# Kernel tuning notes

Hardware: AMD Instinct MI355X
Metric: run time of the kernel (lower is better)

The kernel has to match this reference:

```python
import jax, jax.numpy as jnp
import numpy as np


def setup_inputs() -> dict:
    key = jax.random.key(0)
    ks = jax.random.split(key, 8)
    B = 65536
    scale = lambda fan_in: 1.0 / np.sqrt(fan_in)
    return {
        "x": jax.random.normal(ks[0], (B, 784), dtype=jnp.float32),
        "w0": jax.random.normal(ks[1], (124, 784), dtype=jnp.float32) * scale(784),
        "w1": jax.random.normal(ks[2], (32, 124), dtype=jnp.float32) * scale(124),
        "w3": jax.random.normal(ks[3], (22, 32), dtype=jnp.float32) * scale(32),
        "b3": jax.random.normal(ks[4], (22,), dtype=jnp.float32) * scale(32),
        "w5": jax.random.normal(ks[5], (21, 22), dtype=jnp.float32) * scale(22),
        "b5": jax.random.normal(ks[6], (21,), dtype=jnp.float32) * scale(22),
        "w7": jax.random.normal(ks[7], (10, 21), dtype=jnp.float32) * scale(21),
    }


def reference(x, w0, w1, w3, b3, w5, b5, w7):
    # x: [B, 784]; PyTorch Linear: y = x @ W.T (+ b)
    h = x @ w0.T                       # [B, 124] (no bias, no activation)
    h = jax.nn.relu(h @ w1.T)          # [B, 32]
    h = jax.nn.relu(h @ w3.T + b3)     # [B, 22]
    h = jax.nn.relu(h @ w5.T + b5)     # [B, 21]
    logits = h @ w7.T                  # [B, 10]
    return jax.nn.log_softmax(logits, axis=1)
```

## Files before the change

kernel.cpp:

```cpp
#include <hip/hip_runtime.h>
#include <hip/hip_fp16.h>

typedef _Float16 half8 __attribute__((ext_vector_type(8)));
typedef __fp16 cvt2_t __attribute__((ext_vector_type(2)));
typedef float f32x4 __attribute__((ext_vector_type(4)));

#define W0F_UNITS (13 * 1024)
#define W1F_OFF   (W0F_UNITS * 16)
#define W1F_UNITS 512
#define SW_OFF    (W1F_OFF + W1F_UNITS * 16)

#define L_H0   0
#define L_H1   8192
#define L_H3   0
#define L_H5   3200
#define L_OS   6400
#define LDS_SZ 10240

__global__ void prep_weights(const float* __restrict__ w0,
                             const float* __restrict__ w1,
                             const float* __restrict__ w3,
                             const float* __restrict__ b3,
                             const float* __restrict__ w5,
                             const float* __restrict__ b5,
                             const float* __restrict__ w7,
                             char* __restrict__ ws) {
  int tid = blockIdx.x * 256 + threadIdx.x;
  if (tid < W0F_UNITS) {
    int t  = tid >> 10;
    int kf = (tid >> 9) & 1;
    int nf = (tid >> 6) & 7;
    int l  = tid & 63;
    int n  = nf * 16 + (l & 15);
    int k0 = t * 64 + kf * 32 + (l >> 4) * 8;
    alignas(16) __half h[8];
#pragma unroll
    for (int e = 0; e < 8; e++) {
      int k = k0 + e;
      h[e] = __float2half((n < 124 && k < 784) ? w0[n * 784 + k] : 0.f);
    }
    *(uint4*)(ws + tid * 16) = *(const uint4*)h;
    return;
  }
  int r = tid - W0F_UNITS;
  if (r < W1F_UNITS) {
    int kf = r >> 7;
    int nf = (r >> 6) & 1;
    int l  = r & 63;
    int n  = nf * 16 + (l & 15);
    int k0 = kf * 32 + (l >> 4) * 8;
    alignas(16) __half h[8];
#pragma unroll
    for (int e = 0; e < 8; e++) {
      int k = k0 + e;
      h[e] = __float2half((k < 124) ? w1[n * 124 + k] : 0.f);
    }
    *(uint4*)(ws + W1F_OFF + r * 16) = *(const uint4*)h;
    return;
  }
  r -= W1F_UNITS;
  float* sw = (float*)(ws + SW_OFF);
  if (r < 704) { sw[r] = w3[r]; return; }
  r -= 704;
  if (r < 504) {
    int n = r / 24, k = r % 24;
    sw[704 + r] = (k < 22) ? w5[n * 22 + k] : 0.f;
    return;
  }
  r -= 504;
  if (r < 240) {
    int n = r / 24, k = r % 24;
    sw[1208 + r] = (k < 21) ? w7[n * 21 + k] : 0.f;
    return;
  }
  r -= 240;
  if (r < 24) { sw[1448 + r] = (r < 22) ? b3[r] : 0.f; return; }
  r -= 24;
  if (r < 24) { sw[1472 + r] = (r < 21) ? b5[r] : 0.f; return; }
}

__device__ __forceinline__ half8 cvt8(const f32x4& a, const f32x4& b) {
  cvt2_t p0 = __builtin_amdgcn_cvt_pkrtz(a[0], a[1]);
  cvt2_t p1 = __builtin_amdgcn_cvt_pkrtz(a[2], a[3]);
  cvt2_t p2 = __builtin_amdgcn_cvt_pkrtz(b[0], b[1]);
  cvt2_t p3 = __builtin_amdgcn_cvt_pkrtz(b[2], b[3]);
  uint4 u;
  u.x = __builtin_bit_cast(unsigned, p0);
  u.y = __builtin_bit_cast(unsigned, p1);
  u.z = __builtin_bit_cast(unsigned, p2);
  u.w = __builtin_bit_cast(unsigned, p3);
  return __builtin_bit_cast(half8, u);
}

__global__ __launch_bounds__(64, 2) void fused_mlp(
    const float* __restrict__ x, const char* __restrict__ ws,
    float* __restrict__ out) {
  __shared__ alignas(16) char sm[LDS_SZ];
  const int l  = threadIdx.x;
  const int lr = l & 15;
  const int lg = l >> 4;
  const size_t row0 = (size_t)blockIdx.x * 32;
  const uint4* wf = (const uint4*)ws;

  const float* xb0 = x + (row0 + lr) * 784;
  const float* xb1 = xb0 + 16 * 784;

  f32x4 acc[2][8];
#pragma unroll
  for (int mf = 0; mf < 2; mf++)
#pragma unroll
    for (int nf = 0; nf < 8; nf++) acc[mf][nf] = f32x4{0.f, 0.f, 0.f, 0.f};

  f32x4 xr[2][4][2];
  half8 afr[2][4];
  half8 bfr[2][8];

#define XL(T, G)                                                               \
  {                                                                            \
    _Pragma("unroll") for (int mf = 0; mf < 2; mf++)                           \
        _Pragma("unroll") for (int kf = 0; kf < 4; kf++)                       \
            _Pragma("unroll") for (int h = 0; h < 2; h++) {                    \
      const float* p =                                                         \
          (mf ? xb1 : xb0) + (T) * 128 + kf * 32 + lg * 8 + h * 4;             \
      if (!(G) || (kf == 0 && lg < 2))                                         \
        xr[mf][kf][h] = *(const f32x4*)p;                                      \
      else                                                                     \
        xr[mf][kf][h] = f32x4{0.f, 0.f, 0.f, 0.f};                             \
    }                                                                          \
  }

#define CVALL()                                                                \
  {                                                                            \
    _Pragma("unroll") for (int mf = 0; mf < 2; mf++)                           \
        _Pragma("unroll") for (int kf = 0; kf < 4; kf++)                       \
            afr[mf][kf] = cvt8(xr[mf][kf][0], xr[mf][kf][1]);                  \
  }

#define BFL(P, G)                                                              \
  {                                                                            \
    _Pragma("unroll") for (int nf = 0; nf < 8; nf++)                           \
      bfr[P][nf] = __builtin_bit_cast(                                         \
          half8, wf[((G) >> 1) * 1024 + ((G) & 1) * 512 + nf * 64 + l]);       \
  }

#define MFK(KF, P)                                                             \
  {                                                                            \
    _Pragma("unroll") for (int nf = 0; nf < 8; nf++) {                         \
      acc[0][nf] = __builtin_amdgcn_mfma_f32_16x16x32_f16(                     \
          afr[0][KF], bfr[P][nf], acc[0][nf], 0, 0, 0);                        \
      acc[1][nf] = __builtin_amdgcn_mfma_f32_16x16x32_f16(                     \
          afr[1][KF], bfr[P][nf], acc[1][nf], 0, 0, 0);                        \
    }                                                                          \
  }

#define BODY(T, GN)                                                            \
  {                                                                            \
    CVALL()                                                                    \
    XL((T) + 1, GN)                                                            \
    MFK(0, 0)                                                                  \
    BFL(0, (T) * 4 + 2)                                                        \
    MFK(1, 1)                                                                  \
    BFL(1, (T) * 4 + 3)                                                        \
    MFK(2, 0)                                                                  \
    BFL(0, ((T) + 1) * 4 + 0)                                                  \
    MFK(3, 1)                                                                  \
    BFL(1, ((T) + 1) * 4 + 1)                                                  \
  }

  XL(0, 0)
  BFL(0, 0)
  BFL(1, 1)

  BODY(0, 0)
  BODY(1, 0)
  BODY(2, 0)
  BODY(3, 0)
  BODY(4, 0)
  BODY(5, 1)
  CVALL()
  MFK(0, 0)

  half8 b1[4][2];
  {
    const uint4* w1f = (const uint4*)(ws + W1F_OFF);
#pragma unroll
    for (int kf = 0; kf < 4; kf++)
#pragma unroll
      for (int nf = 0; nf < 2; nf++)
        b1[kf][nf] = __builtin_bit_cast(half8, w1f[kf * 128 + nf * 64 + l]);
  }

#pragma unroll
  for (int mf = 0; mf < 2; mf++)
#pragma unroll
    for (int nf = 0; nf < 8; nf++)
#pragma unroll
      for (int q = 0; q < 4; q++) {
        int rr = mf * 16 + lg * 4 + q;
        int cc = nf * 16 + lr;
        *(__half*)(sm + L_H0 + rr * 256 + ((2 * cc) ^ ((rr & 7) << 4))) =
            __float2half(acc[mf][nf][q]);
      }
  __syncthreads();

  f32x4 acc1[2][2];
#pragma unroll
  for (int mf = 0; mf < 2; mf++) {
    acc1[mf][0] = f32x4{0.f, 0.f, 0.f, 0.f};
    acc1[mf][1] = f32x4{0.f, 0.f, 0.f, 0.f};
  }
#pragma unroll
  for (int kf = 0; kf < 4; kf++) {
    half8 a1[2];
#pragma unroll
    for (int mf = 0; mf < 2; mf++) {
      int rr = mf * 16 + lr;
      int cb = kf * 64 + lg * 16;
      a1[mf] = *(const half8*)(sm + L_H0 + rr * 256 + (cb ^ ((rr & 7) << 4)));
    }
#pragma unroll
    for (int mf = 0; mf < 2; mf++)
#pragma unroll
      for (int nf = 0; nf < 2; nf++)
        acc1[mf][nf] = __builtin_amdgcn_mfma_f32_16x16x32_f16(
            a1[mf], b1[kf][nf], acc1[mf][nf], 0, 0, 0);
  }
#pragma unroll
  for (int mf = 0; mf < 2; mf++)
#pragma unroll
    for (int nf = 0; nf < 2; nf++)
#pragma unroll
      for (int q = 0; q < 4; q++) {
        int rr = mf * 16 + lg * 4 + q;
        int cc = nf * 16 + lr;
        float v = fmaxf(acc1[mf][nf][q], 0.f);
        *(__half*)(sm + L_H1 + rr * 64 + ((2 * cc) ^ ((rr & 3) << 4))) =
            __float2half(v);
      }
  __syncthreads();

  const int r = l & 31;
  const int j = l >> 5;
  float h1v[32];
#pragma unroll
  for (int cb = 0; cb < 4; cb++) {
    half8 v = *(const half8*)(sm + L_H1 + r * 64 + ((cb * 16) ^ ((r & 3) << 4)));
#pragma unroll
    for (int e = 0; e < 8; e++) h1v[cb * 8 + e] = (float)v[e];
  }
  const float* w3g = (const float*)(ws + SW_OFF);
  const float* w5g = (const float*)(ws + SW_OFF + 2816);
  const float* w7g = (const float*)(ws + SW_OFF + 4832);
  const float* b3g = (const float*)(ws + SW_OFF + 5792);
  const float* b5g = (const float*)(ws + SW_OFF + 5888);
  float* h3l = (float*)(sm + L_H3);
  float* h5l = (float*)(sm + L_H5);

#pragma unroll
  for (int i = 0; i < 11; i++) {
    int n = j + 2 * i;
    float s = b3g[n];
    const float4* wrow = (const float4*)(w3g + n * 32);
#pragma unroll
    for (int kk = 0; kk < 8; kk++) {
      float4 wv = wrow[kk];
      s += h1v[4 * kk] * wv.x + h1v[4 * kk + 1] * wv.y +
           h1v[4 * kk + 2] * wv.z + h1v[4 * kk + 3] * wv.w;
    }
    h3l[r * 25 + n] = fmaxf(s, 0.f);
  }
  __syncthreads();
  float h3v[24];
#pragma unroll
  for (int k = 0; k < 24; k++) h3v[k] = (k < 22) ? h3l[r * 25 + k] : 0.f;
#pragma unroll
  for (int i = 0; i < 11; i++) {
    int n = j + 2 * i;
    if (n < 21) {
      float s = b5g[n];
      const float4* wrow = (const float4*)(w5g + n * 24);
#pragma unroll
      for (int kk = 0; kk < 6; kk++) {
        float4 wv = wrow[kk];
        s += h3v[4 * kk] * wv.x + h3v[4 * kk + 1] * wv.y +
             h3v[4 * kk + 2] * wv.z + h3v[4 * kk + 3] * wv.w;
      }
      h5l[r * 25 + n] = fmaxf(s, 0.f);
    }
  }
  __syncthreads();
  if (j == 0) {
    float h5v[24];
#pragma unroll
    for (int k = 0; k < 24; k++) h5v[k] = (k < 21) ? h5l[r * 25 + k] : 0.f;
    float lgt[10];
    float mx = -3.4e38f;
#pragma unroll
    for (int n = 0; n < 10; n++) {
      float s = 0.f;
      const float4* wrow = (const float4*)(w7g + n * 24);
#pragma unroll
      for (int kk = 0; kk < 6; kk++) {
        float4 wv = wrow[kk];
        s += h5v[4 * kk] * wv.x + h5v[4 * kk + 1] * wv.y +
             h5v[4 * kk + 2] * wv.z + h5v[4 * kk + 3] * wv.w;
      }
      lgt[n] = s;
      mx = fmaxf(mx, s);
    }
    float se = 0.f;
#pragma unroll
    for (int n = 0; n < 10; n++) se += __expf(lgt[n] - mx);
    const float lse = mx + __logf(se);
    float* os = (float*)(sm + L_OS);
#pragma unroll
    for (int n = 0; n < 10; n++) os[r * 10 + n] = lgt[n] - lse;
  }
  __syncthreads();
  {
    const float* os = (const float*)(sm + L_OS);
#pragma unroll
    for (int i = 0; i < 5; i++) out[row0 * 10 + i * 64 + l] = os[i * 64 + l];
  }
}

extern "C" void kernel_launch(void* const* d_in, const int* in_sizes, int n_in,
                              void* d_out, int out_size, void* d_ws, size_t ws_size,
                              hipStream_t stream) {
  const float* x  = (const float*)d_in[0];
  const float* w0 = (const float*)d_in[1];
  const float* w1 = (const float*)d_in[2];
  const float* w3 = (const float*)d_in[3];
  const float* b3 = (const float*)d_in[4];
  const float* w5 = (const float*)d_in[5];
  const float* b5 = (const float*)d_in[6];
  const float* w7 = (const float*)d_in[7];
  float* out = (float*)d_out;
  char* ws = (char*)d_ws;

  const int prep_threads = W0F_UNITS + W1F_UNITS + 704 + 504 + 240 + 24 + 24;
  prep_weights<<<(prep_threads + 255) / 256, 256, 0, stream>>>(w0, w1, w3, b3,
                                                               w5, b5, w7, ws);
  fused_mlp<<<65536 / 32, 64, 0, stream>>>(x, ws, out);
}
```

Before: 60.99 us.

## Stage x tiles through swizzled LDS double buffer for coalesced loads

Each lane now loads a contiguous 64-float strip of x across rows, so global reads are coalesced. The tile is converted to fp16 and stored into a double-buffered, XOR-swizzled LDS tile, then A fragments are read back from LDS in MFMA layout. The pipeline moves from 128-wide to 64-wide k-steps with a one-stage prefetch. This adds LDS write and read traffic and a smaller per-iteration MFMA batch in exchange for better global access patterns. There is no explicit barrier, which relies on a single-wavefront block.

```diff
diff --git a/kernel.cpp b/kernel.cpp
--- a/kernel.cpp
+++ b/kernel.cpp
@@ -10,6 +10,8 @@
 #define W1F_UNITS 512
 #define SW_OFF    (W1F_OFF + W1F_UNITS * 16)
 
+#define L_XT0  0
+#define L_XT1  4096
 #define L_H0   0
 #define L_H1   8192
 #define L_H3   0
@@ -79,19 +81,6 @@
   if (r < 24) { sw[1472 + r] = (r < 21) ? b5[r] : 0.f; return; }
 }
 
-__device__ __forceinline__ half8 cvt8(const f32x4& a, const f32x4& b) {
-  cvt2_t p0 = __builtin_amdgcn_cvt_pkrtz(a[0], a[1]);
-  cvt2_t p1 = __builtin_amdgcn_cvt_pkrtz(a[2], a[3]);
-  cvt2_t p2 = __builtin_amdgcn_cvt_pkrtz(b[0], b[1]);
-  cvt2_t p3 = __builtin_amdgcn_cvt_pkrtz(b[2], b[3]);
-  uint4 u;
-  u.x = __builtin_bit_cast(unsigned, p0);
-  u.y = __builtin_bit_cast(unsigned, p1);
-  u.z = __builtin_bit_cast(unsigned, p2);
-  u.w = __builtin_bit_cast(unsigned, p3);
-  return __builtin_bit_cast(half8, u);
-}
-
 __global__ __launch_bounds__(64, 2) void fused_mlp(
     const float* __restrict__ x, const char* __restrict__ ws,
     float* __restrict__ out) {
@@ -102,38 +91,46 @@
   const size_t row0 = (size_t)blockIdx.x * 32;
   const uint4* wf = (const uint4*)ws;
 
-  const float* xb0 = x + (row0 + lr) * 784;
-  const float* xb1 = xb0 + 16 * 784;
-
   f32x4 acc[2][8];
 #pragma unroll
   for (int mf = 0; mf < 2; mf++)
 #pragma unroll
     for (int nf = 0; nf < 8; nf++) acc[mf][nf] = f32x4{0.f, 0.f, 0.f, 0.f};
 
-  f32x4 xr[2][4][2];
-  half8 afr[2][4];
+  f32x4 xr[8];
   half8 bfr[2][8];
+  half8 af[2][2];
 
 #define XL(T, G)                                                               \
   {                                                                            \
+    _Pragma("unroll") for (int i = 0; i < 8; i++) {                            \
+      const int rr = 4 * i + lg;                                               \
+      const float* p = x + (row0 + rr) * 784 + (T) * 64 + lr * 4;              \
+      xr[i] = (!(G) || lr < 4) ? *(const f32x4*)p : f32x4{0.f, 0.f, 0.f, 0.f}; \
+    }                                                                          \
+  }
+
+#define XST(BUF)                                                               \
+  {                                                                            \
+    _Pragma("unroll") for (int i = 0; i < 8; i++) {                            \
+      const int rr = 4 * i + lg;                                               \
+      cvt2_t q0 = __builtin_amdgcn_cvt_pkrtz(xr[i][0], xr[i][1]);              \
+      cvt2_t q1 = __builtin_amdgcn_cvt_pkrtz(xr[i][2], xr[i][3]);              \
+      uint2 u;                                                                 \
+      u.x = __builtin_bit_cast(unsigned, q0);                                  \
+      u.y = __builtin_bit_cast(unsigned, q1);                                  \
+      *(uint2*)(sm + (BUF) + rr * 128 + ((8 * lr) ^ ((rr & 7) << 4))) = u;     \
+    }                                                                          \
+  }
+
+#define ARD(BUF)                                                               \
+  {                                                                            \
     _Pragma("unroll") for (int mf = 0; mf < 2; mf++)                           \
-        _Pragma("unroll") for (int kf = 0; kf < 4; kf++)                       \
-            _Pragma("unroll") for (int h = 0; h < 2; h++) {                    \
-      const float* p =                                                         \
-          (mf ? xb1 : xb0) + (T) * 128 + kf * 32 + lg * 8 + h * 4;             \
-      if (!(G) || (kf == 0 && lg < 2))                                         \
-        xr[mf][kf][h] = *(const f32x4*)p;                                      \
-      else                                                                     \
-        xr[mf][kf][h] = f32x4{0.f, 0.f, 0.f, 0.f};                             \
+        _Pragma("unroll") for (int kf = 0; kf < 2; kf++) {                     \
+      const int rr = lr + mf * 16;                                             \
+      af[mf][kf] = *(const half8*)(                                            \
+          sm + (BUF) + rr * 128 + ((kf * 64 + lg * 16) ^ ((rr & 7) << 4)));    \
     }                                                                          \
-  }
-
-#define CVALL()                                                                \
-  {                                                                            \
-    _Pragma("unroll") for (int mf = 0; mf < 2; mf++)                           \
-        _Pragma("unroll") for (int kf = 0; kf < 4; kf++)                       \
-            afr[mf][kf] = cvt8(xr[mf][kf][0], xr[mf][kf][1]);                  \
   }
 
 #define BFL(P, G)                                                              \
@@ -147,38 +144,42 @@
   {                                                                            \
     _Pragma("unroll") for (int nf = 0; nf < 8; nf++) {                         \
       acc[0][nf] = __builtin_amdgcn_mfma_f32_16x16x32_f16(                     \
-          afr[0][KF], bfr[P][nf], acc[0][nf], 0, 0, 0);                        \
+          af[0][KF], bfr[P][nf], acc[0][nf], 0, 0, 0);                         \
       acc[1][nf] = __builtin_amdgcn_mfma_f32_16x16x32_f16(                     \
-          afr[1][KF], bfr[P][nf], acc[1][nf], 0, 0, 0);                        \
+          af[1][KF], bfr[P][nf], acc[1][nf], 0, 0, 0);                         \
     }                                                                          \
   }
 
-#define BODY(T, GN)                                                            \
-  {                                                                            \
-    CVALL()                                                                    \
-    XL((T) + 1, GN)                                                            \
+#define BODY(T, BUFC, BUFN, DO_STAGE, DO_LOAD, GNEXT)                          \
+  {                                                                            \
+    ARD(BUFC)                                                                  \
     MFK(0, 0)                                                                  \
-    BFL(0, (T) * 4 + 2)                                                        \
+    if (DO_STAGE) BFL(0, 2 * (T) + 2)                                          \
     MFK(1, 1)                                                                  \
-    BFL(1, (T) * 4 + 3)                                                        \
-    MFK(2, 0)                                                                  \
-    BFL(0, ((T) + 1) * 4 + 0)                                                  \
-    MFK(3, 1)                                                                  \
-    BFL(1, ((T) + 1) * 4 + 1)                                                  \
+    if (DO_STAGE) BFL(1, 2 * (T) + 3)                                          \
+    if (DO_STAGE) XST(BUFN)                                                    \
+    if (DO_LOAD) XL((T) + 2, GNEXT)                                            \
   }
 
   XL(0, 0)
   BFL(0, 0)
   BFL(1, 1)
-
-  BODY(0, 0)
-  BODY(1, 0)
-  BODY(2, 0)
-  BODY(3, 0)
-  BODY(4, 0)
-  BODY(5, 1)
-  CVALL()
-  MFK(0, 0)
+  XST(L_XT0)
+  XL(1, 0)
+
+  BODY(0,  L_XT0, L_XT1, 1, 1, 0)
+  BODY(1,  L_XT1, L_XT0, 1, 1, 0)
+  BODY(2,  L_XT0, L_XT1, 1, 1, 0)
+  BODY(3,  L_XT1, L_XT0, 1, 1, 0)
+  BODY(4,  L_XT0, L_XT1, 1, 1, 0)
+  BODY(5,  L_XT1, L_XT0, 1, 1, 0)
+  BODY(6,  L_XT0, L_XT1, 1, 1, 0)
+  BODY(7,  L_XT1, L_XT0, 1, 1, 0)
+  BODY(8,  L_XT0, L_XT1, 1, 1, 0)
+  BODY(9,  L_XT1, L_XT0, 1, 1, 0)
+  BODY(10, L_XT0, L_XT1, 1, 1, 1)
+  BODY(11, L_XT1, L_XT0, 1, 0, 0)
+  BODY(12, L_XT0, L_XT1, 0, 0, 0)
 
   half8 b1[4][2];
   {
```

After: 59.05 us. -3.2%, faster.
